# Performance work log

Measured on AMD Instinct MI355X. Metric: run time of the kernel, lower is better.

## Reference

```python
import jax, jax.numpy as jnp
import numpy as np
import math

B, IN, D, H, DEPTH, E, K = 16384, 128, 512, 8, 3, 8, 2
FF, EH = 4 * D, 256          # ffn width = 4*d_model; expert hidden fixed at 256 in source
EPSILON = 0.1                # forward() default epsilon (exploration mixing)
LN_EPS = 1e-5


def _ln(x, w, b):
    m = x.mean(-1, keepdims=True)
    v = x.var(-1, keepdims=True)  # biased variance, matching nn.LayerNorm
    return (x - m) / jnp.sqrt(v + LN_EPS) * w + b


def setup_inputs() -> dict:
    key = jax.random.key(0)
    ks = jax.random.split(key, 16)
    s = 0.02
    rn = lambda k, shape: jax.random.normal(k, shape, jnp.float32) * s
    return dict(
        x=jax.random.normal(ks[0], (B, IN), jnp.float32),
        embed_w=rn(ks[1], (IN, D)), embed_b=jnp.zeros((D,), jnp.float32),
        ln1_w=jnp.ones((DEPTH, D), jnp.float32), ln1_b=jnp.zeros((DEPTH, D), jnp.float32),
        inproj_w=rn(ks[2], (DEPTH, 3 * D, D)), inproj_b=jnp.zeros((DEPTH, 3 * D), jnp.float32),
        outproj_w=rn(ks[3], (DEPTH, D, D)), outproj_b=jnp.zeros((DEPTH, D), jnp.float32),
        ln2_w=jnp.ones((DEPTH, D), jnp.float32), ln2_b=jnp.zeros((DEPTH, D), jnp.float32),
        ffn_w1=rn(ks[4], (DEPTH, D, FF)), ffn_b1=jnp.zeros((DEPTH, FF), jnp.float32),
        ffn_w2=rn(ks[5], (DEPTH, FF, D)), ffn_b2=jnp.zeros((DEPTH, D), jnp.float32),
        router_w=rn(ks[6], (D, E)), router_b=jnp.zeros((E,), jnp.float32),
        exp_w1=rn(ks[7], (E, D, EH)), exp_b1=jnp.zeros((E, EH), jnp.float32),
        exp_w2=rn(ks[8], (E, EH, D)), exp_b2=jnp.zeros((E, D), jnp.float32),
        head_ln_w=jnp.ones((D,), jnp.float32), head_ln_b=jnp.zeros((D,), jnp.float32),
        head_w=rn(ks[9], (D, 1)), head_b=jnp.zeros((1,), jnp.float32),
    )


def reference(x, embed_w, embed_b, ln1_w, ln1_b, inproj_w, inproj_b,
              outproj_w, outproj_b, ln2_w, ln2_b, ffn_w1, ffn_b1, ffn_w2, ffn_b2,
              router_w, router_b, exp_w1, exp_b1, exp_w2, exp_b2,
              head_ln_w, head_ln_b, head_w, head_b):
    h = x @ embed_w + embed_b                       # [B, D]; unsqueeze(1) -> seq_len == 1
    for l in range(DEPTH):
        g = _ln(h, ln1_w[l], ln1_b[l])
        qkv = g @ inproj_w[l].T + inproj_b[l]       # [B, 3D]
        # seq_len == 1: softmax over the single key is exactly 1, so attn(h,h,h) == out_proj(V)
        v = qkv[:, 2 * D:]
        a = v @ outproj_w[l].T + outproj_b[l]
        h = h + a
        g = _ln(h, ln2_w[l], ln2_b[l])
        h = h + jax.nn.gelu(g @ ffn_w1[l] + ffn_b1[l], approximate=False) @ ffn_w2[l] + ffn_b2[l]
    z = h                                           # squeeze(1)

    # WaggleGate
    logits = z @ router_w + router_b                # [B, E]
    probs = jax.nn.softmax(logits, axis=-1)
    probs = (1.0 - EPSILON) * probs + EPSILON / E
    wts, idx = jax.lax.top_k(probs, K)              # [B, K]
    load = probs.mean(0)
    aux = (load * jnp.log(load * E + 1e-9)).sum() / math.log(E + 1e-9)

    # dense all-expert compute + sparse top-k combine (same math as per-sample dispatch)
    hmid = jax.nn.gelu(jnp.einsum('bd,edh->ebh', z, exp_w1) + exp_b1[:, None, :], approximate=False)
    eo = jnp.einsum('ebh,ehd->ebd', hmid, exp_w2) + exp_b2[:, None, :]   # [E, B, D]
    gate = jnp.zeros((z.shape[0], E), z.dtype).at[
        jnp.arange(z.shape[0])[:, None], idx].add(wts)                    # [B, E]
    moe = jnp.einsum('be,ebd->bd', gate, eo)

    z = z + moe
    logit = (_ln(z, head_ln_w, head_ln_b) @ head_w + head_b)[:, 0]       # [B]
    return logit, aux
```

## Files before the change

### kernel.cpp

```cpp
#include <hip/hip_runtime.h>
#include <hip/hip_bf16.h>

#define B_TOK 16384
#define IN_DIM 128
#define D_DIM 512
#define DEPTH 3
#define NEXP 8
#define FF_DIM 2048
#define EH_DIM 256
#define MAXSLOT 34816
#define MAXT256 136
#define NHBLK 64

typedef __attribute__((ext_vector_type(8))) __bf16 bf16x8;
typedef __attribute__((ext_vector_type(4))) float f32x4;
typedef __attribute__((ext_vector_type(4))) unsigned short u16x4;
typedef __attribute__((ext_vector_type(8))) unsigned short u16x8;

__device__ __forceinline__ unsigned short f2bf(float f){
    unsigned int u = __float_as_uint(f);
    u += 0x7fffu + ((u >> 16) & 1u);
    return (unsigned short)(u >> 16);
}
__device__ __forceinline__ float bf2f(unsigned short u){
    return __uint_as_float(((unsigned int)u) << 16);
}
__device__ __forceinline__ float geluf(float x){
    float x2 = x * x;
    float y  = x * (0.79788456080287f + 0.03567740814183f * x2);
    y = fminf(fmaxf(y, -15.0f), 15.0f);
    float e = __expf(2.0f * y);
    float th = 1.0f - 2.0f / (e + 1.0f);
    return 0.5f * x * (1.0f + th);
}
__device__ __forceinline__ void gload_lds16(const void* g, void* l){
    __builtin_amdgcn_global_load_lds((const __attribute__((address_space(1))) unsigned int*)g,
                                     (__attribute__((address_space(3))) unsigned int*)l,
                                     16, 0, 0);
}
__device__ __forceinline__ int xcd_swizzle(int orig, int nwg){
    const int q = nwg >> 3, r = nwg & 7;
    const int xcd = orig & 7;
    const int idx = orig >> 3;
    return (xcd < r ? xcd*(q+1) : r*(q+1) + (xcd-r)*q) + idx;
}

__global__ void zero_kernel(int* a, int na, int* b, int nb){
    const int i = blockIdx.x * blockDim.x + threadIdx.x;
    if (i < na) a[i] = 0;
    if (i < nb) b[i] = 0;
}

struct ConvSeg { const float* src; unsigned short* dst; int n4; };
struct ConvArgs { ConvSeg seg[2]; };

__global__ void convert_kernel(ConvArgs a){
    const int stride = gridDim.x * blockDim.x;
    const int tid = blockIdx.x * blockDim.x + threadIdx.x;
    for (int s = 0; s < 2; ++s){
        const f32x4* src = (const f32x4*)a.seg[s].src;
        u16x4* dst = (u16x4*)a.seg[s].dst;
        const int n4 = a.seg[s].n4;
        for (int i = tid; i < n4; i += stride){
            f32x4 v = src[i];
            u16x4 o;
            o[0] = f2bf(v[0]); o[1] = f2bf(v[1]); o[2] = f2bf(v[2]); o[3] = f2bf(v[3]);
            dst[i] = o;
        }
    }
}

struct TSeg { const float* src; unsigned short* dst; int K; int N; int tileStart; };
struct TArgs { TSeg seg[26]; };

__global__ void transpose_kernel(TArgs a){
    __shared__ float t[32][33];
    const int tile = blockIdx.x;
    int s = 0;
    #pragma unroll 1
    while (s < 25 && tile >= a.seg[s+1].tileStart) ++s;
    const TSeg sg = a.seg[s];
    const int local = tile - sg.tileStart;
    const int tilesN = sg.N >> 5;
    const int k0 = (local / tilesN) << 5;
    const int n0 = (local % tilesN) << 5;
    const int tx = threadIdx.x & 31;
    const int ty = threadIdx.x >> 5;
    #pragma unroll
    for (int j = 0; j < 4; ++j)
        t[ty + j*8][tx] = sg.src[(size_t)(k0 + ty + j*8) * sg.N + n0 + tx];
    __syncthreads();
    #pragma unroll
    for (int j = 0; j < 4; ++j){
        const int n = ty + j*8;
        sg.dst[(size_t)(n0 + n) * sg.K + k0 + tx] = f2bf(t[tx][n]);
    }
}

__global__ void foldb_kernel(const float* __restrict__ outproj_w, const float* __restrict__ outproj_b,
                             const float* __restrict__ inproj_b, float* __restrict__ bfold){
    const int wave = threadIdx.x >> 6, lane = threadIdx.x & 63;
    const int o = blockIdx.x * 4 + wave;
    const int l = o >> 9, n = o & 511;
    const float* Wo = outproj_w + ((size_t)l*D_DIM + n)*D_DIM;
    const float* bv = inproj_b + l*3*D_DIM + 2*D_DIM;
    float s = 0.f;
    #pragma unroll
    for (int j = 0; j < 8; ++j) s += Wo[lane + j*64] * bv[lane + j*64];
    #pragma unroll
    for (int off = 32; off > 0; off >>= 1) s += __shfl_xor(s, off);
    if (lane == 0) bfold[o] = s + outproj_b[o];
}

__global__ void __launch_bounds__(256, 2)
gemm_bt(const unsigned short* __restrict__ A0, const unsigned short* __restrict__ Bt0,
        const float* __restrict__ bias, unsigned short* __restrict__ out0,
        int NB, int N, int K, int nper, size_t lsa, size_t lsb, size_t lsc)
{
    __shared__ unsigned short sh[32768];
    const int nwg = gridDim.x;
    int wg  = xcd_swizzle(blockIdx.x, nwg);
    const int layer = wg / nper;
    wg -= layer * nper;
    const unsigned short* A  = A0  + (size_t)layer * lsa;
    const unsigned short* Bt = Bt0 + (size_t)layer * lsb;
    unsigned short* out = out0 + (size_t)layer * lsc;
    const int bn  = wg % NB;
    const int bm  = wg / NB;

    const int tid  = threadIdx.x;
    const int lane = tid & 63;
    const int wave = tid >> 6;
    const int wm = (wave >> 1) << 6;
    const int wn = (wave & 1) << 6;

    f32x4 acc[4][4] = {};

    const unsigned short* Abase = A + (size_t)bm * 128 * K;
    const unsigned short* Bbase = Bt + (size_t)bn * 128 * K;
    const int soff = tid * 16;

    auto STAGE = [&](int b, int kt){
        char* Ab = (char*)(sh + b*16384);
        char* Bb = (char*)(sh + b*16384 + 8192);
        #pragma unroll
        for (int s = 0; s < 4; ++s){
            const int off = s*4096 + soff;
            const int row = off >> 7, colb = off & 127;
            gload_lds16((const char*)(Abase + (size_t)row*K + kt) + colb, Ab + off);
        }
        #pragma unroll
        for (int s = 0; s < 4; ++s){
            const int off = s*4096 + soff;
            const int row = off >> 7, colb = off & 127;
            gload_lds16((const char*)(Bbase + (size_t)row*K + kt) + colb, Bb + off);
        }
    };
    auto COMPUTE = [&](int b){
        const unsigned short* Ab = sh + b*16384;
        const unsigned short* Bb = sh + b*16384 + 8192;
        #pragma unroll
        for (int ks = 0; ks < 2; ++ks){
            const int k0 = ks*32 + ((lane>>4)<<3);
            bf16x8 af[4], bfr[4];
            #pragma unroll
            for (int i=0;i<4;i++) af[i]  = *(const bf16x8*)&Ab[(wm + i*16 + (lane&15))*64 + k0];
            #pragma unroll
            for (int j=0;j<4;j++) bfr[j] = *(const bf16x8*)&Bb[(wn + j*16 + (lane&15))*64 + k0];
            #pragma unroll
            for (int i=0;i<4;i++)
                #pragma unroll
                for (int j=0;j<4;j++)
                    acc[i][j] = __builtin_amdgcn_mfma_f32_16x16x32_bf16(af[i], bfr[j], acc[i][j], 0, 0, 0);
        }
    };

    STAGE(0, 0);
    __syncthreads();
    const int nk = K >> 6;
    int cur = 0;
    for (int i = 0; i < nk; ++i){
        if (i + 1 < nk) STAGE(cur ^ 1, (i + 1) << 6);
        COMPUTE(cur);
        __syncthreads();
        cur ^= 1;
    }

    const int r0 = ((lane>>4)<<2);
    const int cc = lane & 15;
    unsigned short* Ct = sh;
    float bcol[4];
    #pragma unroll
    for (int j=0;j<4;j++) bcol[j] = bias[bn*128 + wn + j*16 + cc];
    #pragma unroll
    for (int i=0;i<4;i++)
        #pragma unroll
        for (int r=0;r<4;r++){
            const int rl = wm + i*16 + r0 + r;
            #pragma unroll
            for (int j=0;j<4;j++)
                Ct[rl*128 + wn + j*16 + cc] = f2bf(acc[i][j][r] + bcol[j]);
        }
    __syncthreads();
    const int orow = tid >> 4;
    const int ocol = (tid & 15) * 8;
    #pragma unroll
    for (int p = 0; p < 8; ++p){
        const int row = p*16 + orow;
        *(u16x8*)(&out[(size_t)(bm*128 + row)*N + bn*128 + ocol]) = *(u16x8*)&Ct[row*128 + ocol];
    }
}

__global__ void __launch_bounds__(512, 2)
gemm256sq(const unsigned short* __restrict__ A, const unsigned short* __restrict__ Bt,
          const float* __restrict__ bias, unsigned short* __restrict__ out,
          int NB, int N, int K)
{
    __shared__ __align__(16) char sh[131072];
    const int nwg = gridDim.x;
    const int wg  = xcd_swizzle(blockIdx.x, nwg);
    const int bn  = wg % NB;
    const int bm  = wg / NB;
    const int m0  = bm * 256;
    const int n0  = bn * 256;

    const int tid = threadIdx.x, lane = tid & 63, wave = tid >> 6;
    const int wr = wave >> 2;
    const int wc = wave & 3;

    const int srow = wave*16 + (lane >> 3);
    const int scol = ((lane & 7) ^ (lane >> 3)) * 8;
    const unsigned short* aptr[2][2];
    const unsigned short* bptr[2][2];
    #pragma unroll
    for (int u = 0; u < 2; ++u)
        #pragma unroll
        for (int l = 0; l < 2; ++l){
            aptr[u][l] = A  + (size_t)(m0 + u*128 + srow + l*8) * K + scol;
            bptr[u][l] = Bt + (size_t)(n0 + u*128 + srow + l*8) * K + scol;
        }
    const int sdst = wave*2048 + lane*16;

    int ch[2];
    #pragma unroll
    for (int ks = 0; ks < 2; ++ks)
        ch[ks] = ((((ks<<2) + (lane>>4)) ^ (lane & 7)) << 4);
    const int arow = wr*128 + (lane & 15);
    const int brow = wc*64  + (lane & 15);

    f32x4 acc[8][4] = {};

    auto STAGE = [&](int buf, int kt){
        #pragma unroll
        for (int u = 0; u < 2; ++u)
            #pragma unroll
            for (int l = 0; l < 2; ++l)
                gload_lds16(aptr[u][l] + kt, sh + buf*32768 + u*16384 + l*1024 + sdst);
        #pragma unroll
        for (int u = 0; u < 2; ++u)
            #pragma unroll
            for (int l = 0; l < 2; ++l)
                gload_lds16(bptr[u][l] + kt, sh + 65536 + buf*32768 + u*16384 + l*1024 + sdst);
    };
    auto COMPUTE = [&](int buf){
        bf16x8 bfr[4][2];
        #pragma unroll
        for (int nf = 0; nf < 4; ++nf)
            #pragma unroll
            for (int ks = 0; ks < 2; ++ks)
                bfr[nf][ks] = *(const bf16x8*)(sh + 65536 + buf*32768 + (brow + nf*16)*128 + ch[ks]);
        #pragma unroll
        for (int mf = 0; mf < 8; ++mf){
            bf16x8 af[2];
            #pragma unroll
            for (int ks = 0; ks < 2; ++ks)
                af[ks] = *(const bf16x8*)(sh + buf*32768 + (arow + mf*16)*128 + ch[ks]);
            #pragma unroll
            for (int nf = 0; nf < 4; ++nf)
                #pragma unroll
                for (int ks = 0; ks < 2; ++ks)
                    acc[mf][nf] = __builtin_amdgcn_mfma_f32_16x16x32_bf16(af[ks], bfr[nf][ks], acc[mf][nf], 0,0,0);
        }
    };

    STAGE(0, 0);
    __syncthreads();
    const int nk = K >> 6;
    int cur = 0;
    for (int i = 0; i < nk; ++i){
        if (i + 1 < nk) STAGE(cur ^ 1, (i + 1) << 6);
        COMPUTE(cur);
        __syncthreads();
        cur ^= 1;
    }

    unsigned short* Ct = (unsigned short*)sh;
    const int r4 = (lane >> 4) * 4;
    const int cc = lane & 15;
    #pragma unroll
    for (int nf = 0; nf < 4; ++nf){
        const int col = wc*64 + nf*16 + cc;
        const float bv = bias[n0 + col];
        #pragma unroll
        for (int mf = 0; mf < 8; ++mf)
            #pragma unroll
            for (int r = 0; r < 4; ++r){
                const int row = wr*128 + mf*16 + r4 + r;
                Ct[row*256 + col] = f2bf(geluf(acc[mf][nf][r] + bv));
            }
    }
    __syncthreads();
    #pragma unroll
    for (int p = 0; p < 16; ++p){
        const int uidx = p*512 + tid;
        const int row = uidx >> 5;
        const int cu  = uidx & 31;
        *(u16x8*)(out + (size_t)(m0 + row)*N + n0 + cu*8) = *(const u16x8*)(Ct + row*256 + cu*8);
    }
}

#define G_GELU_BF16 0
#define G_BF16_RESID 1
#define G_GATED_BF16 2

template<int EPI, int MOE, int INDIRECT>
__global__ void __launch_bounds__(512, 2)
gemm256(const unsigned short* __restrict__ A, const unsigned short* __restrict__ BtG,
        const float* __restrict__ biasG, const unsigned short* __restrict__ resid,
        const int* __restrict__ tok, const int* __restrict__ offs,
        int wstride, int bstride, const float* __restrict__ gslot,
        unsigned short* __restrict__ out, int NB, int N, int K)
{
    __shared__ __align__(16) char sh[147456];
    const int nwg = gridDim.x;
    const int wg  = xcd_swizzle(blockIdx.x, nwg);
    const int bn  = wg % NB;
    const int bm  = wg / NB;
    const int m0  = bm * 256;

    const unsigned short* Bt = BtG;
    const float* bias = biasG;
    if (MOE){
        if (m0 >= offs[8]) return;
        int e = 0;
        #pragma unroll 1
        while (offs[e+1] <= m0) ++e;
        Bt   += (size_t)e * wstride;
        bias += (size_t)e * bstride;
    }

    const int tid = threadIdx.x, lane = tid & 63, wave = tid >> 6;
    const int wm = (wave >> 1) * 64;
    const int wn = (wave & 1) * 64;

    const int srow = wave*16 + (lane >> 3);
    const int scol = ((lane & 7) ^ (lane >> 3)) * 8;
    const unsigned short* aptr[2][2];
    #pragma unroll
    for (int u = 0; u < 2; ++u)
        #pragma unroll
        for (int l = 0; l < 2; ++l){
            const int r = u*128 + srow + l*8;
            const int gr = INDIRECT ? tok[m0 + r] : (m0 + r);
            aptr[u][l] = A + (size_t)gr * K + scol;
        }
    const unsigned short* bptr[2];
    #pragma unroll
    for (int l = 0; l < 2; ++l)
        bptr[l] = Bt + (size_t)(bn*128 + srow + l*8) * K + scol;
    const int sdst = wave*2048 + lane*16;

    int aoff[2], boff[2];
    #pragma unroll
    for (int ks = 0; ks < 2; ++ks){
        const int ch = (((ks<<2) + (lane>>4)) ^ (lane & 7)) << 4;
        aoff[ks] = (wm + (lane & 15))*128 + ch;
        boff[ks] = (wn + (lane & 15))*128 + ch;
    }

    f32x4 acc[4][4] = {};

    auto STAGE = [&](int buf, int kt){
        #pragma unroll
        for (int u = 0; u < 2; ++u)
            #pragma unroll
            for (int l = 0; l < 2; ++l)
                gload_lds16(aptr[u][l] + kt, sh + buf*32768 + u*16384 + l*1024 + sdst);
        #pragma unroll
        for (int l = 0; l < 2; ++l)
            gload_lds16(bptr[l] + kt, sh + 98304 + buf*16384 + l*1024 + sdst);
    };
    auto COMPUTE = [&](int buf){
        bf16x8 bfr[4][2];
        #pragma unroll
        for (int nf = 0; nf < 4; ++nf)
            #pragma unroll
            for (int ks = 0; ks < 2; ++ks)
                bfr[nf][ks] = *(const bf16x8*)(sh + 98304 + buf*16384 + nf*2048 + boff[ks]);
        #pragma unroll
        for (int mf = 0; mf < 4; ++mf){
            bf16x8 af[2];
            #pragma unroll
            for (int ks = 0; ks < 2; ++ks)
                af[ks] = *(const bf16x8*)(sh + buf*32768 + mf*2048 + aoff[ks]);
            #pragma unroll
            for (int nf = 0; nf < 4; ++nf)
                #pragma unroll
                for (int ks = 0; ks < 2; ++ks)
                    acc[mf][nf] = __builtin_amdgcn_mfma_f32_16x16x32_bf16(af[ks], bfr[nf][ks], acc[mf][nf], 0,0,0);
        }
    };

    STAGE(0, 0);
    __syncthreads();
    const int nk = K >> 6;
    int cur = 0;
    for (int i = 0; i < nk; ++i){
        if (i + 1 < nk) STAGE(cur ^ 1, (i + 1) << 6);
        COMPUTE(cur);
        __syncthreads();
        cur ^= 1;
    }

    const int r4 = (lane >> 4) * 4;
    const int cc = lane & 15;
    if (EPI == G_BF16_RESID){
        float* ctf = (float*)sh;
        #pragma unroll
        for (int nf = 0; nf < 4; ++nf){
            const float bv = bias[bn*128 + wn + nf*16 + cc];
            #pragma unroll
            for (int mf = 0; mf < 4; ++mf)
                #pragma unroll
                for (int r = 0; r < 4; ++r){
                    const int row = wm + mf*16 + r4 + r;
                    ctf[row*128 + wn + nf*16 + cc] = acc[mf][nf][r] + bv;
                }
        }
        __syncthreads();
        #pragma unroll
        for (int p = 0; p < 8; ++p){
            const int uidx = p*512 + tid;
            const int row = uidx >> 4;
            const int cu  = uidx & 15;
            const size_t gidx = (size_t)(m0 + row)*N + bn*128 + cu*8;
            u16x8 hv = *(const u16x8*)(resid + gidx);
            u16x8 o;
            #pragma unroll
            for (int j = 0; j < 8; ++j)
                o[j] = f2bf(bf2f(hv[j]) + ctf[row*128 + cu*8 + j]);
            *(u16x8*)(out + gidx) = o;
        }
    } else {
        unsigned short* ct = (unsigned short*)sh;
        #pragma unroll
        for (int nf = 0; nf < 4; ++nf){
            const float bv = bias[bn*128 + wn + nf*16 + cc];
            #pragma unroll
            for (int mf = 0; mf < 4; ++mf)
                #pragma unroll
                for (int r = 0; r < 4; ++r){
                    const int row = wm + mf*16 + r4 + r;
                    float v = acc[mf][nf][r] + bv;
                    if (EPI == G_GELU_BF16) v = geluf(v);
                    else                    v *= gslot[m0 + row];
                    ct[row*128 + wn + nf*16 + cc] = f2bf(v);
                }
        }
        __syncthreads();
        #pragma unroll
        for (int p = 0; p < 8; ++p){
            const int uidx = p*512 + tid;
            const int row = uidx >> 4;
            const int cu  = uidx & 15;
            *(u16x8*)(out + (size_t)(m0 + row)*N + bn*128 + cu*8) =
                *(const u16x8*)(ct + row*128 + cu*8);
        }
    }
}

__global__ void ln_kernel(const unsigned short* __restrict__ x, const float* __restrict__ w,
                          const float* __restrict__ b, unsigned short* __restrict__ out)
{
    const int lane = threadIdx.x & 63;
    const int wave = threadIdx.x >> 6;
    const int row  = blockIdx.x * 4 + wave;
    u16x8 hv = *(const u16x8*)(x + (size_t)row * D_DIM + lane*8);
    float v[8];
    #pragma unroll
    for (int j = 0; j < 8; ++j) v[j] = bf2f(hv[j]);
    float s = 0.f, s2 = 0.f;
    #pragma unroll
    for (int j = 0; j < 8; ++j){ s += v[j]; s2 += v[j]*v[j]; }
    #pragma unroll
    for (int o = 32; o > 0; o >>= 1){ s += __shfl_xor(s, o); s2 += __shfl_xor(s2, o); }
    const float mean = s * (1.0f/512.0f);
    const float var  = s2 * (1.0f/512.0f) - mean*mean;
    const float inv  = 1.0f / sqrtf(var + 1e-5f);
    const int k = lane*8;
    u16x8 o;
    #pragma unroll
    for (int j = 0; j < 8; ++j) o[j] = f2bf((v[j]-mean)*inv*w[k+j] + b[k+j]);
    *(u16x8*)(out + (size_t)row*D_DIM + k) = o;
}

__global__ void router_kernel(const unsigned short* __restrict__ z, const float* __restrict__ rw,
                              const float* __restrict__ rb,
                              int2* __restrict__ idx2, float2* __restrict__ wts2,
                              float* __restrict__ bsums)
{
    __shared__ float ps[4][8];
    const int lane = threadIdx.x & 63;
    const int wave = threadIdx.x >> 6;
    const int row  = blockIdx.x * 4 + wave;
    u16x8 hv = *(const u16x8*)(z + (size_t)row * D_DIM + lane*8);
    float acc[8] = {0,0,0,0,0,0,0,0};
    #pragma unroll
    for (int j = 0; j < 8; ++j){
        const float zv = bf2f(hv[j]);
        const float* wr = rw + (size_t)(lane*8 + j) * 8;
        f32x4 w0 = *(const f32x4*)wr;
        f32x4 w1 = *(const f32x4*)(wr + 4);
        acc[0] += zv*w0[0]; acc[1] += zv*w0[1]; acc[2] += zv*w0[2]; acc[3] += zv*w0[3];
        acc[4] += zv*w1[0]; acc[5] += zv*w1[1]; acc[6] += zv*w1[2]; acc[7] += zv*w1[3];
    }
    #pragma unroll
    for (int o = 32; o > 0; o >>= 1){
        #pragma unroll
        for (int e = 0; e < 8; ++e) acc[e] += __shfl_xor(acc[e], o);
    }
    if (lane == 0){
        float p[8]; float mx = -1e30f;
        #pragma unroll
        for (int e=0;e<8;e++){ p[e] = acc[e] + rb[e]; mx = fmaxf(mx, p[e]); }
        float se = 0.f;
        #pragma unroll
        for (int e=0;e<8;e++){ p[e] = expf(p[e]-mx); se += p[e]; }
        const float sc = 0.9f / se;
        #pragma unroll
        for (int e=0;e<8;e++) p[e] = p[e]*sc + 0.0125f;
        int i1 = 0;
        #pragma unroll
        for (int e=1;e<8;e++) if (p[e] > p[i1]) i1 = e;
        int i2 = (i1 == 0) ? 1 : 0;
        for (int e=i2+1;e<8;e++) if (e != i1 && p[e] > p[i2]) i2 = e;
        idx2[row] = make_int2(i1, i2);
        wts2[row] = make_float2(p[i1], p[i2]);
        #pragma unroll
        for (int e=0;e<8;e++) ps[wave][e] = p[e];
    }
    __syncthreads();
    if (threadIdx.x < 8){
        bsums[blockIdx.x*8 + threadIdx.x] =
            ps[0][threadIdx.x] + ps[1][threadIdx.x] + ps[2][threadIdx.x] + ps[3][threadIdx.x];
    }
}
// ... 106 lines not shown
    const float var  = s2 * (1.0f/512.0f) - mean*mean;
    const float inv  = 1.0f / sqrtf(var + 1e-5f);
    const int k = lane*8;
    float dot = 0.f;
    #pragma unroll
    for (int j=0;j<8;j++) dot += ((v[j]-mean)*inv*w[k+j] + b[k+j]) * hw[k+j];
    #pragma unroll
    for (int o = 32; o > 0; o >>= 1) dot += __shfl_xor(dot, o);
    if (lane == 0) out[row] = dot + hb[0];
}

extern "C" void kernel_launch(void* const* d_in, const int* in_sizes, int n_in,
                              void* d_out, int out_size, void* d_ws, size_t ws_size,
                              hipStream_t stream)
{
    (void)in_sizes; (void)n_in; (void)out_size; (void)ws_size;
    const float* x         = (const float*)d_in[0];
    const float* embed_w   = (const float*)d_in[1];
    const float* embed_b   = (const float*)d_in[2];
    const float* ln1_w     = (const float*)d_in[3];
    const float* ln1_b     = (const float*)d_in[4];
    const float* inproj_w  = (const float*)d_in[5];
    const float* inproj_b  = (const float*)d_in[6];
    const float* outproj_w = (const float*)d_in[7];
    const float* outproj_b = (const float*)d_in[8];
    const float* ln2_w     = (const float*)d_in[9];
    const float* ln2_b     = (const float*)d_in[10];
    const float* ffn_w1    = (const float*)d_in[11];
    const float* ffn_b1    = (const float*)d_in[12];
    const float* ffn_w2    = (const float*)d_in[13];
    const float* ffn_b2    = (const float*)d_in[14];
    const float* router_w  = (const float*)d_in[15];
    const float* router_b  = (const float*)d_in[16];
    const float* exp_w1    = (const float*)d_in[17];
    const float* exp_b1    = (const float*)d_in[18];
    const float* exp_w2    = (const float*)d_in[19];
    const float* exp_b2    = (const float*)d_in[20];
    const float* head_ln_w = (const float*)d_in[21];
    const float* head_ln_b = (const float*)d_in[22];
    const float* head_w    = (const float*)d_in[23];
    const float* head_b    = (const float*)d_in[24];

    char* ws = (char*)d_ws;
    unsigned short* xbf   = (unsigned short*)(ws + 0);
    unsigned short* ebf   = (unsigned short*)(ws + 4194304);
    unsigned short* wobf  = (unsigned short*)(ws + 4325376);
    unsigned short* wvtbf = (unsigned short*)(ws + 5898240);
    unsigned short* wfold = (unsigned short*)(ws + 7471104);
    unsigned short* w1t   = (unsigned short*)(ws + 9043968);
    unsigned short* w2t   = (unsigned short*)(ws + 15335424);
    unsigned short* e1t   = (unsigned short*)(ws + 21626880);
    unsigned short* e2t   = (unsigned short*)(ws + 23724032);
    unsigned short* h     = (unsigned short*)(ws + 25821184);
    unsigned short* gbf   = (unsigned short*)(ws + 42598400);
    unsigned short* ubf   = (unsigned short*)(ws + 59375616);
    unsigned short* hmidg = ubf;
    unsigned short* eog   = (unsigned short*)(ws + 77201408);
    char* MISC = ws + 126484480;
    int*    offs     = (int*)(MISC + 0);
    float*  zbias    = (float*)(MISC + 256);
    float*  bfold    = (float*)(MISC + 2304);
    int2*   idx2     = (int2*)(MISC + 8448);
    float2* wts2     = (float2*)(MISC + 139520);
    int2*   slot_map = (int2*)(MISC + 270592);
    float*  gslot    = (float*)(MISC + 401664);
    int*    tok      = (int*)(MISC + 544768);
    float*  bsums    = (float*)(MISC + 684032);
    int*    blockHist= (int*)(MISC + 815104);
    int*    baseArr  = (int*)(MISC + 817152);
    float* out = (float*)d_out;

    zero_kernel<<<(MAXSLOT + 255)/256, 256, 0, stream>>>((int*)zbias, 512, tok, MAXSLOT);

    ConvArgs ca;
    ca.seg[0] = { x, xbf, B_TOK*IN_DIM/4 };
    ca.seg[1] = { outproj_w, wobf, DEPTH*D_DIM*D_DIM/4 };
    convert_kernel<<<1024, 256, 0, stream>>>(ca);

    TArgs ta;
    int tcur = 0, ti = 0;
    ta.seg[ti] = { embed_w, ebf, IN_DIM, D_DIM, tcur };
    tcur += (IN_DIM/32)*(D_DIM/32); ++ti;
    for (int l = 0; l < DEPTH; ++l){
        ta.seg[ti] = { ffn_w1 + (size_t)l*D_DIM*FF_DIM, w1t + (size_t)l*FF_DIM*D_DIM, D_DIM, FF_DIM, tcur };
        tcur += (D_DIM/32)*(FF_DIM/32); ++ti;
    }
    for (int l = 0; l < DEPTH; ++l){
        ta.seg[ti] = { ffn_w2 + (size_t)l*FF_DIM*D_DIM, w2t + (size_t)l*D_DIM*FF_DIM, FF_DIM, D_DIM, tcur };
        tcur += (FF_DIM/32)*(D_DIM/32); ++ti;
    }
    for (int e = 0; e < NEXP; ++e){
        ta.seg[ti] = { exp_w1 + (size_t)e*D_DIM*EH_DIM, e1t + (size_t)e*EH_DIM*D_DIM, D_DIM, EH_DIM, tcur };
        tcur += (D_DIM/32)*(EH_DIM/32); ++ti;
    }
    for (int e = 0; e < NEXP; ++e){
        ta.seg[ti] = { exp_w2 + (size_t)e*EH_DIM*D_DIM, e2t + (size_t)e*D_DIM*EH_DIM, EH_DIM, D_DIM, tcur };
        tcur += (EH_DIM/32)*(D_DIM/32); ++ti;
    }
    for (int l = 0; l < DEPTH; ++l){
        ta.seg[ti] = { inproj_w + (size_t)l*3*D_DIM*D_DIM + 2*D_DIM*D_DIM,
                       wvtbf + (size_t)l*D_DIM*D_DIM, D_DIM, D_DIM, tcur };
        tcur += (D_DIM/32)*(D_DIM/32); ++ti;
    }
    transpose_kernel<<<tcur, 256, 0, stream>>>(ta);

    foldb_kernel<<<DEPTH*D_DIM/4, 256, 0, stream>>>(outproj_w, outproj_b, inproj_b, bfold);

    gemm_bt<<<48, 256, 0, stream>>>(
        wobf, wvtbf, zbias, wfold, 4, D_DIM, D_DIM,
        16, (size_t)D_DIM*D_DIM, (size_t)D_DIM*D_DIM, (size_t)D_DIM*D_DIM);

    gemm_bt<<<(D_DIM/128)*(B_TOK/128), 256, 0, stream>>>(
        xbf, ebf, embed_b, h, D_DIM/128, D_DIM, IN_DIM,
        (D_DIM/128)*(B_TOK/128), 0, 0, 0);

    for (int l = 0; l < DEPTH; ++l){
        ln_kernel<<<B_TOK/4, 256, 0, stream>>>(h, ln1_w + l*D_DIM, ln1_b + l*D_DIM, gbf);
        gemm256<G_BF16_RESID,0,0><<<(B_TOK/256)*(D_DIM/128), 512, 0, stream>>>(
            gbf, wfold + (size_t)l*D_DIM*D_DIM, bfold + l*D_DIM, h,
            nullptr, nullptr, 0, 0, nullptr, h, D_DIM/128, D_DIM, D_DIM);
        ln_kernel<<<B_TOK/4, 256, 0, stream>>>(h, ln2_w + l*D_DIM, ln2_b + l*D_DIM, gbf);
        gemm256sq<<<(B_TOK/256)*(FF_DIM/256), 512, 0, stream>>>(
            gbf, w1t + (size_t)l*FF_DIM*D_DIM, ffn_b1 + l*FF_DIM, ubf, FF_DIM/256, FF_DIM, D_DIM);
        gemm256<G_BF16_RESID,0,0><<<(B_TOK/256)*(D_DIM/128), 512, 0, stream>>>(
            ubf, w2t + (size_t)l*D_DIM*FF_DIM, ffn_b2 + l*D_DIM, h,
            nullptr, nullptr, 0, 0, nullptr, h, D_DIM/128, D_DIM, FF_DIM);
    }

    router_kernel<<<B_TOK/4, 256, 0, stream>>>(h, router_w, router_b, idx2, wts2, bsums);
    aux_kernel<<<1, 256, 0, stream>>>(bsums, out + B_TOK);
    hist_kernel<<<NHBLK, 256, 0, stream>>>(idx2, blockHist);
    scan_kernel<<<1, 512, 0, stream>>>(blockHist, offs, baseArr);
    assign_kernel<<<B_TOK/256, 256, 0, stream>>>(idx2, wts2, baseArr, slot_map, gslot, tok);

    gemm256<G_GELU_BF16,1,1><<<MAXT256*(EH_DIM/128), 512, 0, stream>>>(
        h, e1t, exp_b1, nullptr, tok, offs, EH_DIM*D_DIM, EH_DIM, nullptr,
        hmidg, EH_DIM/128, EH_DIM, D_DIM);
    gemm256<G_GATED_BF16,1,0><<<MAXT256*(D_DIM/128), 512, 0, stream>>>(
        hmidg, e2t, exp_b2, nullptr, nullptr, offs, D_DIM*EH_DIM, D_DIM, gslot,
        eog, D_DIM/128, D_DIM, EH_DIM);

    head_kernel<<<B_TOK/4, 256, 0, stream>>>(h, eog, slot_map, head_ln_w, head_ln_b, head_w, head_b, out);
}
```

Measured before the change: 574.2 us.

## Fold LayerNorm into following GEMMs via row stats and weight prescaling

Replaces the per-layer LayerNorm kernels that wrote a normalized bf16 activation copy with a stats-only kernel that writes per-row (inv, mean*inv). The LN gain is folded into the transposed weights and the LN bias into precomputed column constants. Each GEMM epilogue then applies inv*acc - mean*inv*rowsum(W) + c. This removes the write and re-read of the normalized activations on every layer. The cost is a few small setup kernels, and precision may suffer because raw h is multiplied before mean subtraction, which can cancel badly when the mean is large.

```diff
diff --git a/kernel.cpp b/kernel.cpp
--- a/kernel.cpp
+++ b/kernel.cpp
@@ -70,7 +70,8 @@
     }
 }
 
-struct TSeg { const float* src; unsigned short* dst; int K; int N; int tileStart; };
+struct TSeg { const float* src; unsigned short* dst; int K; int N; int tileStart;
+              const float* scl; int axis; };
 struct TArgs { TSeg seg[26]; };
 
 __global__ void transpose_kernel(TArgs a){
@@ -90,26 +91,78 @@
     for (int j = 0; j < 4; ++j)
         t[ty + j*8][tx] = sg.src[(size_t)(k0 + ty + j*8) * sg.N + n0 + tx];
     __syncthreads();
+    const float sk = (sg.axis == 1) ? sg.scl[k0 + tx] : 1.0f;
     #pragma unroll
     for (int j = 0; j < 4; ++j){
         const int n = ty + j*8;
-        sg.dst[(size_t)(n0 + n) * sg.K + k0 + tx] = f2bf(t[tx][n]);
-    }
-}
-
-__global__ void foldb_kernel(const float* __restrict__ outproj_w, const float* __restrict__ outproj_b,
-                             const float* __restrict__ inproj_b, float* __restrict__ bfold){
+        float v = t[tx][n] * sk;
+        if (sg.axis == 2) v *= sg.scl[n0 + n];
+        sg.dst[(size_t)(n0 + n) * sg.K + k0 + tx] = f2bf(v);
+    }
+}
+
+__global__ void t2_kernel(const float* __restrict__ inproj_w, const float* __restrict__ inproj_b,
+                          const float* __restrict__ ln1_b, float* __restrict__ t2){
+    const int wave = threadIdx.x >> 6, lane = threadIdx.x & 63;
+    const int o = blockIdx.x * 4 + wave;
+    const int l = o >> 9, j = o & 511;
+    const float* Wv = inproj_w + (size_t)l*3*D_DIM*D_DIM + (size_t)2*D_DIM*D_DIM + (size_t)j*D_DIM;
+    const float* b1 = ln1_b + l*D_DIM;
+    float s = 0.f;
+    #pragma unroll
+    for (int q = 0; q < 8; ++q) s += Wv[lane + q*64] * b1[lane + q*64];
+    #pragma unroll
+    for (int off = 32; off > 0; off >>= 1) s += __shfl_xor(s, off);
+    if (lane == 0) t2[o] = s + inproj_b[l*3*D_DIM + 2*D_DIM + j];
+}
+
+__global__ void cca_kernel(const float* __restrict__ outproj_w, const float* __restrict__ outproj_b,
+                           const float* __restrict__ t2, float* __restrict__ cca){
     const int wave = threadIdx.x >> 6, lane = threadIdx.x & 63;
     const int o = blockIdx.x * 4 + wave;
     const int l = o >> 9, n = o & 511;
     const float* Wo = outproj_w + ((size_t)l*D_DIM + n)*D_DIM;
-    const float* bv = inproj_b + l*3*D_DIM + 2*D_DIM;
+    const float* tt = t2 + l*D_DIM;
     float s = 0.f;
     #pragma unroll
-    for (int j = 0; j < 8; ++j) s += Wo[lane + j*64] * bv[lane + j*64];
+    for (int q = 0; q < 8; ++q) s += Wo[lane + q*64] * tt[lane + q*64];
     #pragma unroll
     for (int off = 32; off > 0; off >>= 1) s += __shfl_xor(s, off);
-    if (lane == 0) bfold[o] = s + outproj_b[o];
+    if (lane == 0) cca[o] = s + outproj_b[o];
+}
+
+__global__ void rowsum_kernel(const unsigned short* __restrict__ wfold,
+                              const unsigned short* __restrict__ w1t,
+                              float* __restrict__ c1a, float* __restrict__ c1f){
+    const int wave = threadIdx.x >> 6, lane = threadIdx.x & 63;
+    const int o = blockIdx.x * 4 + wave;
+    const unsigned short* src;
+    float* dst;
+    if (o < DEPTH*D_DIM){ src = wfold + (size_t)o*D_DIM; dst = c1a + o; }
+    else { src = w1t + (size_t)(o - DEPTH*D_DIM)*D_DIM; dst = c1f + (o - DEPTH*D_DIM); }
+    u16x8 v = *(const u16x8*)(src + lane*8);
+    float s = 0.f;
+    #pragma unroll
+    for (int q = 0; q < 8; ++q) s += bf2f(v[q]);
+    #pragma unroll
+    for (int off = 32; off > 0; off >>= 1) s += __shfl_xor(s, off);
+    if (lane == 0) *dst = s;
+}
+
+__global__ void ccf_kernel(const float* __restrict__ ffn_w1, const float* __restrict__ ffn_b1,
+                           const float* __restrict__ ln2_b, float* __restrict__ ccf){
+    __shared__ float lb[512];
+    const int l = blockIdx.x >> 3;
+    const int n0 = (blockIdx.x & 7) * 256;
+    const int t = threadIdx.x;
+    lb[t] = ln2_b[l*D_DIM + t];
+    lb[t + 256] = ln2_b[l*D_DIM + t + 256];
+    __syncthreads();
+    const float* W = ffn_w1 + (size_t)l*D_DIM*FF_DIM;
+    float acc = 0.f;
+    #pragma unroll 1
+    for (int k = 0; k < D_DIM; ++k) acc += lb[k] * W[(size_t)k*FF_DIM + n0 + t];
+    ccf[l*FF_DIM + n0 + t] = acc + ffn_b1[l*FF_DIM + n0 + t];
 }
 
 __global__ void __launch_bounds__(256, 2)
@@ -213,7 +266,8 @@
 
 __global__ void __launch_bounds__(512, 2)
 gemm256sq(const unsigned short* __restrict__ A, const unsigned short* __restrict__ Bt,
-          const float* __restrict__ bias, unsigned short* __restrict__ out,
+          const float* __restrict__ cc, const float* __restrict__ c1,
+          const float2* __restrict__ mr, unsigned short* __restrict__ out,
           int NB, int N, int K)
 {
     __shared__ __align__(16) char sh[131072];
@@ -296,19 +350,26 @@
 
     unsigned short* Ct = (unsigned short*)sh;
     const int r4 = (lane >> 4) * 4;
-    const int cc = lane & 15;
+    const int cc15 = lane & 15;
+    float c1v[4], ccv[4];
     #pragma unroll
     for (int nf = 0; nf < 4; ++nf){
-        const int col = wc*64 + nf*16 + cc;
-        const float bv = bias[n0 + col];
-        #pragma unroll
-        for (int mf = 0; mf < 8; ++mf)
-            #pragma unroll
-            for (int r = 0; r < 4; ++r){
-                const int row = wr*128 + mf*16 + r4 + r;
-                Ct[row*256 + col] = f2bf(geluf(acc[mf][nf][r] + bv));
+        const int col = n0 + wc*64 + nf*16 + cc15;
+        c1v[nf] = c1[col];
+        ccv[nf] = cc[col];
+    }
+    #pragma unroll
+    for (int mf = 0; mf < 8; ++mf)
+        #pragma unroll
+        for (int r = 0; r < 4; ++r){
+            const int row = wr*128 + mf*16 + r4 + r;
+            const float2 m = mr[m0 + row];
+            #pragma unroll
+            for (int nf = 0; nf < 4; ++nf){
+                const int col = wc*64 + nf*16 + cc15;
+                Ct[row*256 + col] = f2bf(geluf(m.x*acc[mf][nf][r] - m.y*c1v[nf] + ccv[nf]));
             }
-    }
+        }
     __syncthreads();
     #pragma unroll
     for (int p = 0; p < 16; ++p){
@@ -322,6 +383,7 @@
 #define G_GELU_BF16 0
 #define G_BF16_RESID 1
 #define G_GATED_BF16 2
+#define G_LNRESID 3
 
 template<int EPI, int MOE, int INDIRECT>
 __global__ void __launch_bounds__(512, 2)
@@ -329,6 +391,7 @@
         const float* __restrict__ biasG, const unsigned short* __restrict__ resid,
         const int* __restrict__ tok, const int* __restrict__ offs,
         int wstride, int bstride, const float* __restrict__ gslot,
+        const float2* __restrict__ mr, const float* __restrict__ c1,
         unsigned short* __restrict__ out, int NB, int N, int K)
 {
     __shared__ __align__(16) char sh[147456];
@@ -423,20 +486,30 @@
     }
 
     const int r4 = (lane >> 4) * 4;
-    const int cc = lane & 15;
-    if (EPI == G_BF16_RESID){
+    const int cc15 = lane & 15;
+    if (EPI == G_BF16_RESID || EPI == G_LNRESID){
         float* ctf = (float*)sh;
+        float bcol[4], c1v[4];
         #pragma unroll
         for (int nf = 0; nf < 4; ++nf){
-            const float bv = bias[bn*128 + wn + nf*16 + cc];
-            #pragma unroll
-            for (int mf = 0; mf < 4; ++mf)
+            bcol[nf] = bias[bn*128 + wn + nf*16 + cc15];
+            if (EPI == G_LNRESID) c1v[nf] = c1[bn*128 + wn + nf*16 + cc15];
+        }
+        #pragma unroll
+        for (int mf = 0; mf < 4; ++mf)
+            #pragma unroll
+            for (int r = 0; r < 4; ++r){
+                const int row = wm + mf*16 + r4 + r;
+                float2 m = make_float2(1.f, 0.f);
+                if (EPI == G_LNRESID) m = mr[m0 + row];
                 #pragma unroll
-                for (int r = 0; r < 4; ++r){
-                    const int row = wm + mf*16 + r4 + r;
-                    ctf[row*128 + wn + nf*16 + cc] = acc[mf][nf][r] + bv;
+                for (int nf = 0; nf < 4; ++nf){
+                    float v;
+                    if (EPI == G_LNRESID) v = m.x*acc[mf][nf][r] - m.y*c1v[nf] + bcol[nf];
+                    else                  v = acc[mf][nf][r] + bcol[nf];
+                    ctf[row*128 + wn + nf*16 + cc15] = v;
                 }
-        }
+            }
         __syncthreads();
         #pragma unroll
         for (int p = 0; p < 8; ++p){
@@ -455,7 +528,7 @@
         unsigned short* ct = (unsigned short*)sh;
         #pragma unroll
         for (int nf = 0; nf < 4; ++nf){
-            const float bv = bias[bn*128 + wn + nf*16 + cc];
+            const float bv = bias[bn*128 + wn + nf*16 + cc15];
             #pragma unroll
             for (int mf = 0; mf < 4; ++mf)
                 #pragma unroll
@@ -464,7 +537,7 @@
                     float v = acc[mf][nf][r] + bv;
                     if (EPI == G_GELU_BF16) v = geluf(v);
                     else                    v *= gslot[m0 + row];
-                    ct[row*128 + wn + nf*16 + cc] = f2bf(v);
+                    ct[row*128 + wn + nf*16 + cc15] = f2bf(v);
                 }
         }
         __syncthreads();
@@ -479,29 +552,23 @@
     }
 }
 
-__global__ void ln_kernel(const unsigned short* __restrict__ x, const float* __restrict__ w,
-                          const float* __restrict__ b, unsigned short* __restrict__ out)
+__global__ void stats_kernel(const unsigned short* __restrict__ x, float2* __restrict__ mr)
 {
     const int lane = threadIdx.x & 63;
     const int wave = threadIdx.x >> 6;
     const int row  = blockIdx.x * 4 + wave;
     u16x8 hv = *(const u16x8*)(x + (size_t)row * D_DIM + lane*8);
-    float v[8];
-    #pragma unroll
-    for (int j = 0; j < 8; ++j) v[j] = bf2f(hv[j]);
     float s = 0.f, s2 = 0.f;
     #pragma unroll
-    for (int j = 0; j < 8; ++j){ s += v[j]; s2 += v[j]*v[j]; }
+    for (int j = 0; j < 8; ++j){ const float v = bf2f(hv[j]); s += v; s2 += v*v; }
     #pragma unroll
     for (int o = 32; o > 0; o >>= 1){ s += __shfl_xor(s, o); s2 += __shfl_xor(s2, o); }
-    const float mean = s * (1.0f/512.0f);
-    const float var  = s2 * (1.0f/512.0f) - mean*mean;
-    const float inv  = 1.0f / sqrtf(var + 1e-5f);
-    const int k = lane*8;
-    u16x8 o;
-    #pragma unroll
-    for (int j = 0; j < 8; ++j) o[j] = f2bf((v[j]-mean)*inv*w[k+j] + b[k+j]);
-    *(u16x8*)(out + (size_t)row*D_DIM + k) = o;
+    if (lane == 0){
+        const float mean = s * (1.0f/512.0f);
+        const float var  = s2 * (1.0f/512.0f) - mean*mean;
+        const float inv  = 1.0f / sqrtf(var + 1e-5f);
+        mr[row] = make_float2(inv, mean*inv);
+    }
 }
 
 __global__ void router_kernel(const unsigned short* __restrict__ z, const float* __restrict__ rw,
@@ -714,14 +781,12 @@
     unsigned short* e1t   = (unsigned short*)(ws + 21626880);
     unsigned short* e2t   = (unsigned short*)(ws + 23724032);
     unsigned short* h     = (unsigned short*)(ws + 25821184);
-    unsigned short* gbf   = (unsigned short*)(ws + 42598400);
     unsigned short* ubf   = (unsigned short*)(ws + 59375616);
     unsigned short* hmidg = ubf;
     unsigned short* eog   = (unsigned short*)(ws + 77201408);
     char* MISC = ws + 126484480;
     int*    offs     = (int*)(MISC + 0);
     float*  zbias    = (float*)(MISC + 256);
-    float*  bfold    = (float*)(MISC + 2304);
     int2*   idx2     = (int2*)(MISC + 8448);
     float2* wts2     = (float2*)(MISC + 139520);
     int2*   slot_map = (int2*)(MISC + 270592);
@@ -730,6 +795,12 @@
     float*  bsums    = (float*)(MISC + 684032);
     int*    blockHist= (int*)(MISC + 815104);
     int*    baseArr  = (int*)(MISC + 817152);
+    float2* mr       = (float2*)(MISC + 860160);
+    float*  t2buf    = (float*)(MISC + 991232);
+    float*  cca      = (float*)(MISC + 997376);
+    float*  c1a      = (float*)(MISC + 1003520);
+    float*  c1f      = (float*)(MISC + 1009664);
+    float*  ccf      = (float*)(MISC + 1034240);
     float* out = (float*)d_out;
 
     zero_kernel<<<(MAXSLOT + 255)/256, 256, 0, stream>>>((int*)zbias, 512, tok, MAXSLOT);
@@ -741,52 +812,63 @@
 
     TArgs ta;
     int tcur = 0, ti = 0;
-    ta.seg[ti] = { embed_w, ebf, IN_DIM, D_DIM, tcur };
+    ta.seg[ti] = { embed_w, ebf, IN_DIM, D_DIM, tcur, nullptr, 0 };
     tcur += (IN_DIM/32)*(D_DIM/32); ++ti;
     for (int l = 0; l < DEPTH; ++l){
-        ta.seg[ti] = { ffn_w1 + (size_t)l*D_DIM*FF_DIM, w1t + (size_t)l*FF_DIM*D_DIM, D_DIM, FF_DIM, tcur };
+        ta.seg[ti] = { ffn_w1 + (size_t)l*D_DIM*FF_DIM, w1t + (size_t)l*FF_DIM*D_DIM,
+                       D_DIM, FF_DIM, tcur, ln2_w + l*D_DIM, 1 };
         tcur += (D_DIM/32)*(FF_DIM/32); ++ti;
     }
     for (int l = 0; l < DEPTH; ++l){
-        ta.seg[ti] = { ffn_w2 + (size_t)l*FF_DIM*D_DIM, w2t + (size_t)l*D_DIM*FF_DIM, FF_DIM, D_DIM, tcur };
+        ta.seg[ti] = { ffn_w2 + (size_t)l*FF_DIM*D_DIM, w2t + (size_t)l*D_DIM*FF_DIM,
+                       FF_DIM, D_DIM, tcur, nullptr, 0 };
         tcur += (FF_DIM/32)*(D_DIM/32); ++ti;
     }
     for (int e = 0; e < NEXP; ++e){
-        ta.seg[ti] = { exp_w1 + (size_t)e*D_DIM*EH_DIM, e1t + (size_t)e*EH_DIM*D_DIM, D_DIM, EH_DIM, tcur };
+        ta.seg[ti] = { exp_w1 + (size_t)e*D_DIM*EH_DIM, e1t + (size_t)e*EH_DIM*D_DIM,
+                       D_DIM, EH_DIM, tcur, nullptr, 0 };
         tcur += (D_DIM/32)*(EH_DIM/32); ++ti;
     }
     for (int e = 0; e < NEXP; ++e){
-        ta.seg[ti] = { exp_w2 + (size_t)e*EH_DIM*D_DIM, e2t + (size_t)e*D_DIM*EH_DIM, EH_DIM, D_DIM, tcur };
+        ta.seg[ti] = { exp_w2 + (size_t)e*EH_DIM*D_DIM, e2t + (size_t)e*D_DIM*EH_DIM,
+                       EH_DIM, D_DIM, tcur, nullptr, 0 };
         tcur += (EH_DIM/32)*(D_DIM/32); ++ti;
     }
     for (int l = 0; l < DEPTH; ++l){
         ta.seg[ti] = { inproj_w + (size_t)l*3*D_DIM*D_DIM + 2*D_DIM*D_DIM,
-                       wvtbf + (size_t)l*D_DIM*D_DIM, D_DIM, D_DIM, tcur };
+                       wvtbf + (size_t)l*D_DIM*D_DIM, D_DIM, D_DIM, tcur, ln1_w + l*D_DIM, 2 };
         tcur += (D_DIM/32)*(D_DIM/32); ++ti;
     }
     transpose_kernel<<<tcur, 256, 0, stream>>>(ta);
 
-    foldb_kernel<<<DEPTH*D_DIM/4, 256, 0, stream>>>(outproj_w, outproj_b, inproj_b, bfold);
+    t2_kernel<<<DEPTH*D_DIM/4, 256, 0, stream>>>(inproj_w, inproj_b, ln1_b, t2buf);
+    cca_kernel<<<DEPTH*D_DIM/4, 256, 0, stream>>>(outproj_w, outproj_b, t2buf, cca);
+    ccf_kernel<<<DEPTH*8, 256, 0, stream>>>(ffn_w1, ffn_b1, ln2_b, ccf);
 
     gemm_bt<<<48, 256, 0, stream>>>(
         wobf, wvtbf, zbias, wfold, 4, D_DIM, D_DIM,
         16, (size_t)D_DIM*D_DIM, (size_t)D_DIM*D_DIM, (size_t)D_DIM*D_DIM);
 
+    rowsum_kernel<<<(DEPTH*D_DIM + DEPTH*FF_DIM)/4, 256, 0, stream>>>(wfold, w1t, c1a, c1f);
+
     gemm_bt<<<(D_DIM/128)*(B_TOK/128), 256, 0, stream>>>(
         xbf, ebf, embed_b, h, D_DIM/128, D_DIM, IN_DIM,
         (D_DIM/128)*(B_TOK/128), 0, 0, 0);
 
     for (int l = 0; l < DEPTH; ++l){
-        ln_kernel<<<B_TOK/4, 256, 0, stream>>>(h, ln1_w + l*D_DIM, ln1_b + l*D_DIM, gbf);
-        gemm256<G_BF16_RESID,0,0><<<(B_TOK/256)*(D_DIM/128), 512, 0, stream>>>(
-            gbf, wfold + (size_t)l*D_DIM*D_DIM, bfold + l*D_DIM, h,
-            nullptr, nullptr, 0, 0, nullptr, h, D_DIM/128, D_DIM, D_DIM);
-        ln_kernel<<<B_TOK/4, 256, 0, stream>>>(h, ln2_w + l*D_DIM, ln2_b + l*D_DIM, gbf);
+        stats_kernel<<<B_TOK/4, 256, 0, stream>>>(h, mr);
+        gemm256<G_LNRESID,0,0><<<(B_TOK/256)*(D_DIM/128), 512, 0, stream>>>(
+            h, wfold + (size_t)l*D_DIM*D_DIM, cca + l*D_DIM, h,
+            nullptr, nullptr, 0, 0, nullptr, mr, c1a + l*D_DIM,
+            h, D_DIM/128, D_DIM, D_DIM);
+        stats_kernel<<<B_TOK/4, 256, 0, stream>>>(h, mr);
         gemm256sq<<<(B_TOK/256)*(FF_DIM/256), 512, 0, stream>>>(
-            gbf, w1t + (size_t)l*FF_DIM*D_DIM, ffn_b1 + l*FF_DIM, ubf, FF_DIM/256, FF_DIM, D_DIM);
+            h, w1t + (size_t)l*FF_DIM*D_DIM, ccf + l*FF_DIM, c1f + l*FF_DIM, mr,
+            ubf, FF_DIM/256, FF_DIM, D_DIM);
         gemm256<G_BF16_RESID,0,0><<<(B_TOK/256)*(D_DIM/128), 512, 0, stream>>>(
             ubf, w2t + (size_t)l*D_DIM*FF_DIM, ffn_b2 + l*D_DIM, h,
-            nullptr, nullptr, 0, 0, nullptr, h, D_DIM/128, D_DIM, FF_DIM);
+            nullptr, nullptr, 0, 0, nullptr, nullptr, nullptr,
+            h, D_DIM/128, D_DIM, FF_DIM);
     }
 
     router_kernel<<<B_TOK/4, 256, 0, stream>>>(h, router_w, router_b, idx2, wts2, bsums);
@@ -797,10 +879,10 @@
 
     gemm256<G_GELU_BF16,1,1><<<MAXT256*(EH_DIM/128), 512, 0, stream>>>(
         h, e1t, exp_b1, nullptr, tok, offs, EH_DIM*D_DIM, EH_DIM, nullptr,
-        hmidg, EH_DIM/128, EH_DIM, D_DIM);
+        nullptr, nullptr, hmidg, EH_DIM/128, EH_DIM, D_DIM);
     gemm256<G_GATED_BF16,1,0><<<MAXT256*(D_DIM/128), 512, 0, stream>>>(
         hmidg, e2t, exp_b2, nullptr, nullptr, offs, D_DIM*EH_DIM, D_DIM, gslot,
-        eog, D_DIM/128, D_DIM, EH_DIM);
+        nullptr, nullptr, eog, D_DIM/128, D_DIM, EH_DIM);
 
     head_kernel<<<B_TOK/4, 256, 0, stream>>>(h, eog, slot_map, head_ln_w, head_ln_b, head_w, head_b, out);
 }
```

Result: slower. 699.1 us (+21.8%).

## Single-buffer LDS in 256-row GEMMs to raise occupancy, split epilogue in halves

Applied to the files above, without the earlier changes.

Drops double-buffered LDS staging in both 256-row GEMM kernels and cuts shared memory to 64KB, with launch bounds raised to 4 blocks per CU. The epilogue now writes the output tile in two 128-row halves so it fits the smaller LDS. The aim is to hide load latency with more resident workgroups instead of in-kernel prefetch. In exchange, each k-step now waits on its load with an extra barrier, so loads no longer overlap compute inside a block. The accumulators (128 floats per thread in gemm256sq) may not fit the register budget at 4 blocks per CU and could spill.

```diff
diff --git a/kernel.cpp b/kernel.cpp
--- a/kernel.cpp
+++ b/kernel.cpp
@@ -211,12 +211,12 @@
     }
 }
 
-__global__ void __launch_bounds__(512, 2)
+__global__ void __launch_bounds__(512, 4)
 gemm256sq(const unsigned short* __restrict__ A, const unsigned short* __restrict__ Bt,
           const float* __restrict__ bias, unsigned short* __restrict__ out,
           int NB, int N, int K)
 {
-    __shared__ __align__(16) char sh[131072];
+    __shared__ __align__(16) char sh[65536];
     const int nwg = gridDim.x;
     const int wg  = xcd_swizzle(blockIdx.x, nwg);
     const int bn  = wg % NB;
@@ -250,31 +250,31 @@
 
     f32x4 acc[8][4] = {};
 
-    auto STAGE = [&](int buf, int kt){
+    auto STAGE = [&](int kt){
         #pragma unroll
         for (int u = 0; u < 2; ++u)
             #pragma unroll
             for (int l = 0; l < 2; ++l)
-                gload_lds16(aptr[u][l] + kt, sh + buf*32768 + u*16384 + l*1024 + sdst);
+                gload_lds16(aptr[u][l] + kt, sh + u*16384 + l*1024 + sdst);
         #pragma unroll
         for (int u = 0; u < 2; ++u)
             #pragma unroll
             for (int l = 0; l < 2; ++l)
-                gload_lds16(bptr[u][l] + kt, sh + 65536 + buf*32768 + u*16384 + l*1024 + sdst);
+                gload_lds16(bptr[u][l] + kt, sh + 32768 + u*16384 + l*1024 + sdst);
     };
-    auto COMPUTE = [&](int buf){
+    auto COMPUTE = [&](){
         bf16x8 bfr[4][2];
         #pragma unroll
         for (int nf = 0; nf < 4; ++nf)
             #pragma unroll
             for (int ks = 0; ks < 2; ++ks)
-                bfr[nf][ks] = *(const bf16x8*)(sh + 65536 + buf*32768 + (brow + nf*16)*128 + ch[ks]);
+                bfr[nf][ks] = *(const bf16x8*)(sh + 32768 + (brow + nf*16)*128 + ch[ks]);
         #pragma unroll
         for (int mf = 0; mf < 8; ++mf){
             bf16x8 af[2];
             #pragma unroll
             for (int ks = 0; ks < 2; ++ks)
-                af[ks] = *(const bf16x8*)(sh + buf*32768 + (arow + mf*16)*128 + ch[ks]);
+                af[ks] = *(const bf16x8*)(sh + (arow + mf*16)*128 + ch[ks]);
             #pragma unroll
             for (int nf = 0; nf < 4; ++nf)
                 #pragma unroll
@@ -283,39 +283,43 @@
         }
     };
 
-    STAGE(0, 0);
-    __syncthreads();
     const int nk = K >> 6;
-    int cur = 0;
     for (int i = 0; i < nk; ++i){
-        if (i + 1 < nk) STAGE(cur ^ 1, (i + 1) << 6);
-        COMPUTE(cur);
+        STAGE(i << 6);
         __syncthreads();
-        cur ^= 1;
+        COMPUTE();
+        __syncthreads();
     }
 
     unsigned short* Ct = (unsigned short*)sh;
     const int r4 = (lane >> 4) * 4;
     const int cc = lane & 15;
-    #pragma unroll
-    for (int nf = 0; nf < 4; ++nf){
-        const int col = wc*64 + nf*16 + cc;
-        const float bv = bias[n0 + col];
-        #pragma unroll
-        for (int mf = 0; mf < 8; ++mf)
-            #pragma unroll
-            for (int r = 0; r < 4; ++r){
-                const int row = wr*128 + mf*16 + r4 + r;
-                Ct[row*256 + col] = f2bf(geluf(acc[mf][nf][r] + bv));
+    float bcol[4];
+    #pragma unroll
+    for (int nf = 0; nf < 4; ++nf) bcol[nf] = bias[n0 + wc*64 + nf*16 + cc];
+    #pragma unroll
+    for (int half = 0; half < 2; ++half){
+        if (wr == half){
+            #pragma unroll
+            for (int nf = 0; nf < 4; ++nf){
+                const int col = wc*64 + nf*16 + cc;
+                #pragma unroll
+                for (int mf = 0; mf < 8; ++mf)
+                    #pragma unroll
+                    for (int r = 0; r < 4; ++r)
+                        Ct[(mf*16 + r4 + r)*256 + col] = f2bf(geluf(acc[mf][nf][r] + bcol[nf]));
             }
-    }
-    __syncthreads();
-    #pragma unroll
-    for (int p = 0; p < 16; ++p){
-        const int uidx = p*512 + tid;
-        const int row = uidx >> 5;
-        const int cu  = uidx & 31;
-        *(u16x8*)(out + (size_t)(m0 + row)*N + n0 + cu*8) = *(const u16x8*)(Ct + row*256 + cu*8);
+        }
+        __syncthreads();
+        #pragma unroll
+        for (int p = 0; p < 8; ++p){
+            const int uidx = p*512 + tid;
+            const int row = uidx >> 5;
+            const int cu  = uidx & 31;
+            *(u16x8*)(out + (size_t)(m0 + half*128 + row)*N + n0 + cu*8) =
+                *(const u16x8*)(Ct + row*256 + cu*8);
+        }
+        __syncthreads();
     }
 }
 
@@ -324,14 +328,14 @@
 #define G_GATED_BF16 2
 
 template<int EPI, int MOE, int INDIRECT>
-__global__ void __launch_bounds__(512, 2)
+__global__ void __launch_bounds__(512, 4)
 gemm256(const unsigned short* __restrict__ A, const unsigned short* __restrict__ BtG,
         const float* __restrict__ biasG, const unsigned short* __restrict__ resid,
         const int* __restrict__ tok, const int* __restrict__ offs,
         int wstride, int bstride, const float* __restrict__ gslot,
         unsigned short* __restrict__ out, int NB, int N, int K)
 {
-    __shared__ __align__(16) char sh[147456];
+    __shared__ __align__(16) char sh[65536];
     const int nwg = gridDim.x;
     const int wg  = xcd_swizzle(blockIdx.x, nwg);
     const int bn  = wg % NB;
@@ -380,29 +384,29 @@
 
     f32x4 acc[4][4] = {};
 
-    auto STAGE = [&](int buf, int kt){
+    auto STAGE = [&](int kt){
         #pragma unroll
         for (int u = 0; u < 2; ++u)
             #pragma unroll
             for (int l = 0; l < 2; ++l)
-                gload_lds16(aptr[u][l] + kt, sh + buf*32768 + u*16384 + l*1024 + sdst);
+                gload_lds16(aptr[u][l] + kt, sh + u*16384 + l*1024 + sdst);
         #pragma unroll
         for (int l = 0; l < 2; ++l)
-            gload_lds16(bptr[l] + kt, sh + 98304 + buf*16384 + l*1024 + sdst);
+            gload_lds16(bptr[l] + kt, sh + 32768 + l*1024 + sdst);
     };
-    auto COMPUTE = [&](int buf){
+    auto COMPUTE = [&](){
         bf16x8 bfr[4][2];
         #pragma unroll
         for (int nf = 0; nf < 4; ++nf)
             #pragma unroll
             for (int ks = 0; ks < 2; ++ks)
-                bfr[nf][ks] = *(const bf16x8*)(sh + 98304 + buf*16384 + nf*2048 + boff[ks]);
+                bfr[nf][ks] = *(const bf16x8*)(sh + 32768 + nf*2048 + boff[ks]);
         #pragma unroll
         for (int mf = 0; mf < 4; ++mf){
             bf16x8 af[2];
             #pragma unroll
             for (int ks = 0; ks < 2; ++ks)
-                af[ks] = *(const bf16x8*)(sh + buf*32768 + mf*2048 + aoff[ks]);
+                af[ks] = *(const bf16x8*)(sh + mf*2048 + aoff[ks]);
             #pragma unroll
             for (int nf = 0; nf < 4; ++nf)
                 #pragma unroll
@@ -411,57 +415,62 @@
         }
     };
 
-    STAGE(0, 0);
-    __syncthreads();
     const int nk = K >> 6;
-    int cur = 0;
     for (int i = 0; i < nk; ++i){
-        if (i + 1 < nk) STAGE(cur ^ 1, (i + 1) << 6);
-        COMPUTE(cur);
+        STAGE(i << 6);
         __syncthreads();
-        cur ^= 1;
+        COMPUTE();
+        __syncthreads();
     }
 
     const int r4 = (lane >> 4) * 4;
     const int cc = lane & 15;
     if (EPI == G_BF16_RESID){
         float* ctf = (float*)sh;
+        float bcol[4];
+        #pragma unroll
+        for (int nf = 0; nf < 4; ++nf) bcol[nf] = bias[bn*128 + wn + nf*16 + cc];
+        #pragma unroll
+        for (int half = 0; half < 2; ++half){
+            if ((wm >> 7) == half){
+                const int wml = wm & 127;
+                #pragma unroll
+                for (int nf = 0; nf < 4; ++nf)
+                    #pragma unroll
+                    for (int mf = 0; mf < 4; ++mf)
+                        #pragma unroll
+                        for (int r = 0; r < 4; ++r)
+                            ctf[(wml + mf*16 + r4 + r)*128 + wn + nf*16 + cc] = acc[mf][nf][r] + bcol[nf];
+            }
+            __syncthreads();
+            #pragma unroll
+            for (int p = 0; p < 4; ++p){
+                const int uidx = p*512 + tid;
+                const int row = uidx >> 4;
+                const int cu  = uidx & 15;
+                const size_t gidx = (size_t)(m0 + half*128 + row)*N + bn*128 + cu*8;
+                u16x8 hv = *(const u16x8*)(resid + gidx);
+                u16x8 o;
+                #pragma unroll
+                for (int j = 0; j < 8; ++j)
+                    o[j] = f2bf(bf2f(hv[j]) + ctf[row*128 + cu*8 + j]);
+                *(u16x8*)(out + gidx) = o;
+            }
+            __syncthreads();
+        }
+    } else {
+        unsigned short* ct = (unsigned short*)sh;
+        float bcol[4];
+        #pragma unroll
+        for (int nf = 0; nf < 4; ++nf) bcol[nf] = bias[bn*128 + wn + nf*16 + cc];
         #pragma unroll
         for (int nf = 0; nf < 4; ++nf){
-            const float bv = bias[bn*128 + wn + nf*16 + cc];
             #pragma unroll
             for (int mf = 0; mf < 4; ++mf)
                 #pragma unroll
                 for (int r = 0; r < 4; ++r){
                     const int row = wm + mf*16 + r4 + r;
-                    ctf[row*128 + wn + nf*16 + cc] = acc[mf][nf][r] + bv;
-                }
-        }
-        __syncthreads();
-        #pragma unroll
-        for (int p = 0; p < 8; ++p){
-            const int uidx = p*512 + tid;
-            const int row = uidx >> 4;
-            const int cu  = uidx & 15;
-            const size_t gidx = (size_t)(m0 + row)*N + bn*128 + cu*8;
-            u16x8 hv = *(const u16x8*)(resid + gidx);
-            u16x8 o;
-            #pragma unroll
-            for (int j = 0; j < 8; ++j)
-                o[j] = f2bf(bf2f(hv[j]) + ctf[row*128 + cu*8 + j]);
-            *(u16x8*)(out + gidx) = o;
-        }
-    } else {
-        unsigned short* ct = (unsigned short*)sh;
-        #pragma unroll
-        for (int nf = 0; nf < 4; ++nf){
-            const float bv = bias[bn*128 + wn + nf*16 + cc];
-            #pragma unroll
-            for (int mf = 0; mf < 4; ++mf)
-                #pragma unroll
-                for (int r = 0; r < 4; ++r){
-                    const int row = wm + mf*16 + r4 + r;
-                    float v = acc[mf][nf][r] + bv;
+                    float v = acc[mf][nf][r] + bcol[nf];
                     if (EPI == G_GELU_BF16) v = geluf(v);
                     else                    v *= gslot[m0 + row];
                     ct[row*128 + wn + nf*16 + cc] = f2bf(v);
```

Result: slower. 1.314 ms (+128.8%).
